# Kernel tuning notes

Hardware: AMD Instinct MI355X
Metric: run time of the kernel (lower is better)

## Reference

```python
import jax, jax.numpy as jnp
import numpy as np

B, S, IN = 1, 50000, 128
N = B * S
E = 800000
HID, HEADS, OUT = 64, 2, 64
NEG_SLOPE = 0.2
BN_EPS = 1e-5


def setup_inputs() -> dict:
    key = jax.random.key(0)
    ks = jax.random.split(key, 12)
    s = 0.1
    return {
        "data": jax.random.normal(ks[0], (B, S, IN), jnp.float32),
        "edge_index": jax.random.randint(ks[1], (2, E), 0, N, dtype=jnp.int64),
        "W0": jax.random.normal(ks[2], (IN, HEADS * HID), jnp.float32) * s,
        "att_src0": jax.random.normal(ks[3], (HEADS, HID), jnp.float32) * s,
        "att_dst0": jax.random.normal(ks[4], (HEADS, HID), jnp.float32) * s,
        "bias0": jnp.zeros((HEADS * HID,), jnp.float32),
        "gamma0": jnp.ones((HEADS * HID,), jnp.float32),
        "beta0": jnp.zeros((HEADS * HID,), jnp.float32),
        "W1": jax.random.normal(ks[5], (HEADS * HID, OUT), jnp.float32) * s,
        "att_src1": jax.random.normal(ks[6], (1, OUT), jnp.float32) * s,
        "att_dst1": jax.random.normal(ks[7], (1, OUT), jnp.float32) * s,
        "bias1": jnp.zeros((OUT,), jnp.float32),
    }


def gat_conv(x, edge_index, W, att_src, att_dst, bias, heads, ch, concat):
    n = x.shape[0]
    loop = jnp.arange(n, dtype=edge_index.dtype)
    src = jnp.concatenate([edge_index[0], loop])  # PyG adds self-loops by default
    dst = jnp.concatenate([edge_index[1], loop])
    h = (x @ W).reshape(n, heads, ch)  # [N,H,C]
    a_src = (h * att_src).sum(-1)  # [N,H]
    a_dst = (h * att_dst).sum(-1)  # [N,H]
    e = jax.nn.leaky_relu(a_src[src] + a_dst[dst], NEG_SLOPE)  # [Etot,H]
    m = jax.ops.segment_max(e, dst, num_segments=n)  # segment softmax over dst
    ex = jnp.exp(e - m[dst])
    denom = jax.ops.segment_sum(ex, dst, num_segments=n)
    alpha = ex / (denom[dst] + 1e-16)  # [Etot,H]
    out = jax.ops.segment_sum(h[src] * alpha[:, :, None], dst, num_segments=n)  # [N,H,C]
    out = out.reshape(n, heads * ch) if concat else out.mean(axis=1)
    return out + bias


def reference(data, edge_index, W0, att_src0, att_dst0, bias0, gamma0, beta0,
              W1, att_src1, att_dst1, bias1):
    x = data.reshape(N, IN)
    x = gat_conv(x, edge_index, W0, att_src0, att_dst0, bias0, HEADS, HID, True)
    mu = x.mean(axis=0)
    var = x.var(axis=0)
    x = (x - mu) * jax.lax.rsqrt(var + BN_EPS) * gamma0 + beta0  # BatchNorm1d (batch stats)
    x = jax.nn.elu(x)
    x = gat_conv(x, edge_index, W1, att_src1, att_dst1, bias1, 1, OUT, False)
    return x.reshape(B, S, OUT)
```

## Files before the change

### kernel.cpp

```cpp
#include <hip/hip_runtime.h>
#include <hip/hip_fp16.h>
#include <math.h>

#define N_NODES 50000
#define E_EDGES 800000
#define NEG_SLOPE 0.2f
#define BN_EPS 1e-5f

#define BK_SHIFT 9
#define NBK 98
#define L1_BLOCKS 256
#define L1_CHUNK (E_EDGES / L1_BLOCKS)
#define CNT_N (NBK * L1_BLOCKS)
#define SCG_BLOCKS ((CNT_N + 1023) / 1024)
#define STAGE_MAX 9216

__device__ __forceinline__ float lrelu(float v) { return v > 0.f ? v : NEG_SLOPE * v; }

__global__ void k_zero(float* __restrict__ bn_sum, float* __restrict__ bn_sumsq) {
  int t = threadIdx.x;
  if (t < 128) { bn_sum[t] = 0.f; bn_sumsq[t] = 0.f; }
}

__global__ __launch_bounds__(256) void k_l1hist(const int* __restrict__ dst,
                                                int* __restrict__ cnt) {
  __shared__ int lcnt[NBK];
  int t = threadIdx.x;
  if (t < NBK) lcnt[t] = 0;
  __syncthreads();
  int beg = blockIdx.x * L1_CHUNK, end = beg + L1_CHUNK;
  for (int e = beg + t; e < end; e += 256)
    atomicAdd(&lcnt[((unsigned int)dst[e]) >> BK_SHIFT], 1);
  __syncthreads();
  for (int b = t; b < NBK; b += 256) cnt[b * L1_BLOCKS + blockIdx.x] = lcnt[b];
}

__global__ __launch_bounds__(256) void k_scan1g(const int* __restrict__ cnt,
                                                int* __restrict__ tmp,
                                                int* __restrict__ bsums) {
  __shared__ int ts[256];
  int t = threadIdx.x;
  int base = blockIdx.x * 1024 + t * 4;
  int c0 = (base + 0 < CNT_N) ? cnt[base + 0] : 0;
  int c1 = (base + 1 < CNT_N) ? cnt[base + 1] : 0;
  int c2 = (base + 2 < CNT_N) ? cnt[base + 2] : 0;
  int c3 = (base + 3 < CNT_N) ? cnt[base + 3] : 0;
  int s = c0 + c1 + c2 + c3;
  ts[t] = s;
  __syncthreads();
  for (int off = 1; off < 256; off <<= 1) {
    int v = (t >= off) ? ts[t - off] : 0;
    __syncthreads();
    ts[t] += v;
    __syncthreads();
  }
  int excl = ts[t] - s;
  if (t == 255) bsums[blockIdx.x] = ts[255];
  if (base + 0 < CNT_N) tmp[base + 0] = excl;
  if (base + 1 < CNT_N) tmp[base + 1] = excl + c0;
  if (base + 2 < CNT_N) tmp[base + 2] = excl + c0 + c1;
  if (base + 3 < CNT_N) tmp[base + 3] = excl + c0 + c1 + c2;
}

__global__ void k_scan2g(int* __restrict__ bsums) {
  int t = threadIdx.x;
  int orig = (t < SCG_BLOCKS) ? bsums[t] : 0;
  int v = orig;
#pragma unroll
  for (int off = 1; off < 64; off <<= 1) {
    int u = __shfl_up(v, off);
    if (t >= off) v += u;
  }
  if (t < SCG_BLOCKS) bsums[t] = v - orig;
}

__global__ __launch_bounds__(256) void k_l1scatter(const int* __restrict__ src,
                                                   const int* __restrict__ dst,
                                                   const int* __restrict__ tmp,
                                                   const int* __restrict__ bsums,
                                                   unsigned int* __restrict__ binned) {
  __shared__ int cur[NBK];
  int t = threadIdx.x;
  for (int b = t; b < NBK; b += 256) {
    int idx = b * L1_BLOCKS + blockIdx.x;
    cur[b] = tmp[idx] + bsums[idx >> 10];
  }
  __syncthreads();
  int beg = blockIdx.x * L1_CHUNK, end = beg + L1_CHUNK;
  for (int e = beg + t; e < end; e += 256) {
    unsigned int d = (unsigned int)dst[e];
    int b = d >> BK_SHIFT;
    int p = atomicAdd(&cur[b], 1);
    binned[p] = ((unsigned int)src[e] << 16) | d;
  }
}

__global__ void k_bbase(const int* __restrict__ tmp, const int* __restrict__ bsums,
                        int* __restrict__ bucket_base) {
  int b = threadIdx.x;
  if (b < NBK) {
    int idx = b * L1_BLOCKS;
    bucket_base[b] = tmp[idx] + bsums[idx >> 10];
  }
  if (b == NBK) bucket_base[NBK] = E_EDGES;
}

__global__ __launch_bounds__(256) void k_scatter3(const int* __restrict__ bucket_base,
                                                  const unsigned int* __restrict__ binned,
                                                  int* __restrict__ row_ptr,
                                                  int* __restrict__ csr_src) {
  __shared__ int cnt[512];
  __shared__ int staging[STAGE_MAX];
  __shared__ int ts[256];
  int t = threadIdx.x;
  int b = blockIdx.x;
  int lo = b << BK_SHIFT;
  int hi = lo + 512; if (hi > N_NODES) hi = N_NODES;
  int nloc = hi - lo;
  int base = bucket_base[b];
  int end = bucket_base[b + 1];
  cnt[t] = 0; cnt[t + 256] = 0;
  __syncthreads();
  for (int i = base + t; i < end; i += 256)
    atomicAdd(&cnt[(binned[i] & 0xFFFFu) - lo], 1);
  __syncthreads();
  int c0 = cnt[2 * t], c1 = cnt[2 * t + 1];
  int pair = c0 + c1;
  ts[t] = pair;
  __syncthreads();
  for (int off = 1; off < 256; off <<= 1) {
    int v = (t >= off) ? ts[t - off] : 0;
    __syncthreads();
    ts[t] += v;
    __syncthreads();
  }
  int exclp = ts[t] - pair;
  cnt[2 * t] = exclp;
  cnt[2 * t + 1] = exclp + c0;
  if (2 * t < nloc) row_ptr[lo + 2 * t] = base + exclp;
  if (2 * t + 1 < nloc) row_ptr[lo + 2 * t + 1] = base + exclp + c0;
  if (b == NBK - 1 && t == 0) row_ptr[N_NODES] = E_EDGES;
  __syncthreads();
  for (int i = base + t; i < end; i += 256) {
    unsigned int v = binned[i];
    int d = (int)(v & 0xFFFFu) - lo;
    int p = atomicAdd(&cnt[d], 1);
    int s = (int)(v >> 16);
    if (p < STAGE_MAX) staging[p] = s;
    else csr_src[base + p] = s;
  }
  __syncthreads();
  int tot = end - base;
  int lim = tot < STAGE_MAX ? tot : STAGE_MAX;
  for (int k = t; k < lim; k += 256) csr_src[base + k] = staging[k];
}

__global__ __launch_bounds__(256) void k_gemm0(
    const float* __restrict__ x, const float* __restrict__ W,
    const float* __restrict__ att_s, const float* __restrict__ att_d,
    __half* __restrict__ h, float* __restrict__ a_src, float* __restrict__ a_dst) {
  __shared__ float xs[64 * 132];
  int t = threadIdx.x;
  int rowBase = blockIdx.x * 64;
#pragma unroll
  for (int j = 0; j < 8; j++) {
    int id = t + 256 * j;
    int row = id >> 5;
    int kk = (id & 31) * 4;
    float4 v = make_float4(0.f, 0.f, 0.f, 0.f);
    int gr = rowBase + row;
    if (gr < N_NODES) v = *(const float4*)&x[(size_t)gr * 128 + kk];
    *(float4*)&xs[row * 132 + kk] = v;
  }
  __syncthreads();

  int tc = t & 31, tr = t >> 5;
  int c = tc * 4, r0 = tr * 8;
  float acc[8][4];
#pragma unroll
  for (int i = 0; i < 8; i++)
#pragma unroll
    for (int j = 0; j < 4; j++) acc[i][j] = 0.f;

  for (int k4 = 0; k4 < 128; k4 += 4) {
    float4 wv[4];
#pragma unroll
    for (int kk = 0; kk < 4; kk++) wv[kk] = *(const float4*)&W[(k4 + kk) * 128 + c];
    float4 xv[8];
#pragma unroll
    for (int i = 0; i < 8; i++) xv[i] = *(const float4*)&xs[(r0 + i) * 132 + k4];
#pragma unroll
    for (int i = 0; i < 8; i++) {
      acc[i][0] += xv[i].x * wv[0].x + xv[i].y * wv[1].x + xv[i].z * wv[2].x + xv[i].w * wv[3].x;
      acc[i][1] += xv[i].x * wv[0].y + xv[i].y * wv[1].y + xv[i].z * wv[2].y + xv[i].w * wv[3].y;
      acc[i][2] += xv[i].x * wv[0].z + xv[i].y * wv[1].z + xv[i].z * wv[2].z + xv[i].w * wv[3].z;
      acc[i][3] += xv[i].x * wv[0].w + xv[i].y * wv[1].w + xv[i].z * wv[2].w + xv[i].w * wv[3].w;
    }
  }

  float as4[4], ad4[4];
#pragma unroll
  for (int j = 0; j < 4; j++) { as4[j] = att_s[c + j]; ad4[j] = att_d[c + j]; }
  int head = tc >> 4;
#pragma unroll
  for (int i = 0; i < 8; i++) {
    int gr = rowBase + r0 + i;
    float ps = acc[i][0] * as4[0] + acc[i][1] * as4[1] + acc[i][2] * as4[2] + acc[i][3] * as4[3];
    float pd = acc[i][0] * ad4[0] + acc[i][1] * ad4[1] + acc[i][2] * ad4[2] + acc[i][3] * ad4[3];
#pragma unroll
    for (int msk = 1; msk <= 8; msk <<= 1) {
      ps += __shfl_xor(ps, msk);
      pd += __shfl_xor(pd, msk);
    }
    if (gr < N_NODES) {
      __half2 p01 = __floats2half2_rn(acc[i][0], acc[i][1]);
      __half2 p23 = __floats2half2_rn(acc[i][2], acc[i][3]);
      uint2 pk;
      pk.x = *(unsigned int*)&p01;
      pk.y = *(unsigned int*)&p23;
      *(uint2*)&h[(size_t)gr * 128 + c] = pk;
      if ((t & 15) == 0) {
        a_src[gr * 2 + head] = ps;
        a_dst[gr * 2 + head] = pd;
      }
    }
  }
}

__global__ __launch_bounds__(256) void k_agg0(
    const int* __restrict__ row_ptr, const int* __restrict__ csr_src,
    const __half* __restrict__ h, const float* __restrict__ a_src,
    const float* __restrict__ a_dst, const float* __restrict__ bias,
    float* __restrict__ out) {
  int node = (blockIdx.x * blockDim.x + threadIdx.x) >> 6;
  if (node >= N_NODES) return;
  int l = threadIdx.x & 63;
  int head = l >> 5;
  int c = l * 2;
  float ad = a_dst[node * 2 + head];
  float m = lrelu(a_src[node * 2 + head] + ad);
  float d = 1.f;
  float2 hv = __half22float2(*(const __half2*)&h[(size_t)node * 128 + c]);
  float acc0 = hv.x, acc1 = hv.y;
  int beg = row_ptr[node], end = row_ptr[node + 1];
  int i = beg;
  for (; i + 8 <= end; i += 8) {
    int s0 = csr_src[i], s1 = csr_src[i + 1], s2 = csr_src[i + 2], s3 = csr_src[i + 3];
    int s4 = csr_src[i + 4], s5 = csr_src[i + 5], s6 = csr_src[i + 6], s7 = csr_src[i + 7];
    float e0 = lrelu(a_src[s0 * 2 + head] + ad), e1 = lrelu(a_src[s1 * 2 + head] + ad);
    float e2 = lrelu(a_src[s2 * 2 + head] + ad), e3 = lrelu(a_src[s3 * 2 + head] + ad);
    float e4 = lrelu(a_src[s4 * 2 + head] + ad), e5 = lrelu(a_src[s5 * 2 + head] + ad);
    float e6 = lrelu(a_src[s6 * 2 + head] + ad), e7 = lrelu(a_src[s7 * 2 + head] + ad);
    __half2 p0 = *(const __half2*)&h[(size_t)s0 * 128 + c];
    __half2 p1 = *(const __half2*)&h[(size_t)s1 * 128 + c];
    __half2 p2 = *(const __half2*)&h[(size_t)s2 * 128 + c];
    __half2 p3 = *(const __half2*)&h[(size_t)s3 * 128 + c];
    __half2 p4 = *(const __half2*)&h[(size_t)s4 * 128 + c];
    __half2 p5 = *(const __half2*)&h[(size_t)s5 * 128 + c];
    __half2 p6 = *(const __half2*)&h[(size_t)s6 * 128 + c];
    __half2 p7 = *(const __half2*)&h[(size_t)s7 * 128 + c];
    float nm = fmaxf(m, fmaxf(fmaxf(fmaxf(e0, e1), fmaxf(e2, e3)),
                              fmaxf(fmaxf(e4, e5), fmaxf(e6, e7))));
    float sc = __expf(m - nm);
    float w0 = __expf(e0 - nm), w1 = __expf(e1 - nm), w2 = __expf(e2 - nm), w3 = __expf(e3 - nm);
    float w4 = __expf(e4 - nm), w5 = __expf(e5 - nm), w6 = __expf(e6 - nm), w7 = __expf(e7 - nm);
    d = d * sc + ((w0 + w1) + (w2 + w3)) + ((w4 + w5) + (w6 + w7));
    float2 f0 = __half22float2(p0), f1 = __half22float2(p1);
    float2 f2 = __half22float2(p2), f3 = __half22float2(p3);
    float2 f4 = __half22float2(p4), f5 = __half22float2(p5);
    float2 f6 = __half22float2(p6), f7 = __half22float2(p7);
    acc0 = acc0 * sc + (w0 * f0.x + w1 * f1.x + w2 * f2.x + w3 * f3.x) +
           (w4 * f4.x + w5 * f5.x + w6 * f6.x + w7 * f7.x);
    acc1 = acc1 * sc + (w0 * f0.y + w1 * f1.y + w2 * f2.y + w3 * f3.y) +
           (w4 * f4.y + w5 * f5.y + w6 * f6.y + w7 * f7.y);
    m = nm;
  }
  for (; i + 4 <= end; i += 4) {
    int s0 = csr_src[i], s1 = csr_src[i + 1], s2 = csr_src[i + 2], s3 = csr_src[i + 3];
    float e0 = lrelu(a_src[s0 * 2 + head] + ad), e1 = lrelu(a_src[s1 * 2 + head] + ad);
    float e2 = lrelu(a_src[s2 * 2 + head] + ad), e3 = lrelu(a_src[s3 * 2 + head] + ad);
    __half2 p0 = *(const __half2*)&h[(size_t)s0 * 128 + c];
    __half2 p1 = *(const __half2*)&h[(size_t)s1 * 128 + c];
    __half2 p2 = *(const __half2*)&h[(size_t)s2 * 128 + c];
    __half2 p3 = *(const __half2*)&h[(size_t)s3 * 128 + c];
    float nm = fmaxf(fmaxf(m, e0), fmaxf(fmaxf(e1, e2), e3));
    float sc = __expf(m - nm);
    float w0 = __expf(e0 - nm), w1 = __expf(e1 - nm), w2 = __expf(e2 - nm), w3 = __expf(e3 - nm);
    d = d * sc + (w0 + w1) + (w2 + w3);
    float2 f0 = __half22float2(p0), f1 = __half22float2(p1);
    float2 f2 = __half22float2(p2), f3 = __half22float2(p3);
    acc0 = acc0 * sc + w0 * f0.x + w1 * f1.x + w2 * f2.x + w3 * f3.x;
    acc1 = acc1 * sc + w0 * f0.y + w1 * f1.y + w2 * f2.y + w3 * f3.y;
    m = nm;
  }
  for (; i < end; i++) {
    int s = csr_src[i];
    float ee = lrelu(a_src[s * 2 + head] + ad);
    __half2 pp = *(const __half2*)&h[(size_t)s * 128 + c];
    float nm = fmaxf(m, ee);
    float sc = __expf(m - nm);
    float w = __expf(ee - nm);
    float2 ff = __half22float2(pp);
    d = d * sc + w;
    acc0 = acc0 * sc + w * ff.x;
    acc1 = acc1 * sc + w * ff.y;
    m = nm;
  }
  float inv = 1.f / d;
  float2 o;
  o.x = acc0 * inv + bias[c];
  o.y = acc1 * inv + bias[c + 1];
  *(float2*)&out[(size_t)node * 128 + c] = o;
}

__global__ __launch_bounds__(256) void k_bnstats(const float* __restrict__ x,
                                                 float* __restrict__ bn_sum,
                                                 float* __restrict__ bn_sumsq) {
  int f = threadIdx.x & 127;
  int half = threadIdx.x >> 7;
  float s = 0.f, s2 = 0.f;
  for (int r = blockIdx.x * 2 + half; r < N_NODES; r += gridDim.x * 2) {
    float v = x[(size_t)r * 128 + f];
    s += v;
    s2 += v * v;
  }
  __shared__ float ls[256], ls2[256];
  ls[threadIdx.x] = s;
  ls2[threadIdx.x] = s2;
  __syncthreads();
  if (half == 0) {
    atomicAdd(&bn_sum[f], s + ls[f + 128]);
    atomicAdd(&bn_sumsq[f], s2 + ls2[f + 128]);
  }
}

__global__ void k_bnfinal(const float* __restrict__ sum, const float* __restrict__ sumsq,
                          const float* __restrict__ gamma, const float* __restrict__ beta,
                          float* __restrict__ scale, float* __restrict__ shift) {
  int f = threadIdx.x;
  float mu = sum[f] / (float)N_NODES;
  float var = sumsq[f] / (float)N_NODES - mu * mu;
  float sc = gamma[f] * rsqrtf(var + BN_EPS);
  scale[f] = sc;
  shift[f] = beta[f] - mu * sc;
}

__global__ __launch_bounds__(256) void k_gemm1(
    const float* __restrict__ x, const float* __restrict__ W,
    const float* __restrict__ scale, const float* __restrict__ shift,
    const float* __restrict__ att_s, const float* __restrict__ att_d,
    __half* __restrict__ h, float* __restrict__ a_src, float* __restrict__ a_dst) {
  __shared__ float xs[64 * 132];
  int t = threadIdx.x;
  int rowBase = blockIdx.x * 64;
#pragma unroll
  for (int j = 0; j < 8; j++) {
    int id = t + 256 * j;
    int row = id >> 5;
    int kk = (id & 31) * 4;
    float4 v = make_float4(0.f, 0.f, 0.f, 0.f);
    int gr = rowBase + row;
    if (gr < N_NODES) {
      float4 raw = *(const float4*)&x[(size_t)gr * 128 + kk];
      float4 sc = *(const float4*)&scale[kk];
      float4 sh = *(const float4*)&shift[kk];
      v.x = raw.x * sc.x + sh.x;
      v.y = raw.y * sc.y + sh.y;
      v.z = raw.z * sc.z + sh.z;
      v.w = raw.w * sc.w + sh.w;
      v.x = v.x > 0.f ? v.x : __expf(v.x) - 1.f;
      v.y = v.y > 0.f ? v.y : __expf(v.y) - 1.f;
      v.z = v.z > 0.f ? v.z : __expf(v.z) - 1.f;
      v.w = v.w > 0.f ? v.w : __expf(v.w) - 1.f;
    }
    *(float4*)&xs[row * 132 + kk] = v;
  }
  __syncthreads();

  int tc = t & 15, tr = t >> 4;
  int c = tc * 4, r0 = tr * 4;
  float acc[4][4];
#pragma unroll
  for (int i = 0; i < 4; i++)
#pragma unroll
    for (int j = 0; j < 4; j++) acc[i][j] = 0.f;

  for (int k4 = 0; k4 < 128; k4 += 4) {
    float4 wv[4];
#pragma unroll
    for (int kk = 0; kk < 4; kk++) wv[kk] = *(const float4*)&W[(k4 + kk) * 64 + c];
    float4 xv[4];
#pragma unroll
    for (int i = 0; i < 4; i++) xv[i] = *(const float4*)&xs[(r0 + i) * 132 + k4];
#pragma unroll
    for (int i = 0; i < 4; i++) {
      acc[i][0] += xv[i].x * wv[0].x + xv[i].y * wv[1].x + xv[i].z * wv[2].x + xv[i].w * wv[3].x;
      acc[i][1] += xv[i].x * wv[0].y + xv[i].y * wv[1].y + xv[i].z * wv[2].y + xv[i].w * wv[3].y;
      acc[i][2] += xv[i].x * wv[0].z + xv[i].y * wv[1].z + xv[i].z * wv[2].z + xv[i].w * wv[3].z;
      acc[i][3] += xv[i].x * wv[0].w + xv[i].y * wv[1].w + xv[i].z * wv[2].w + xv[i].w * wv[3].w;
    }
  }

  float as4[4], ad4[4];
#pragma unroll
  for (int j = 0; j < 4; j++) { as4[j] = att_s[c + j]; ad4[j] = att_d[c + j]; }
#pragma unroll
  for (int i = 0; i < 4; i++) {
    int gr = rowBase + r0 + i;
    float ps = acc[i][0] * as4[0] + acc[i][1] * as4[1] + acc[i][2] * as4[2] + acc[i][3] * as4[3];
    float pd = acc[i][0] * ad4[0] + acc[i][1] * ad4[1] + acc[i][2] * ad4[2] + acc[i][3] * ad4[3];
#pragma unroll
    for (int msk = 1; msk <= 8; msk <<= 1) {
      ps += __shfl_xor(ps, msk);
      pd += __shfl_xor(pd, msk);
    }
    if (gr < N_NODES) {
      __half2 p01 = __floats2half2_rn(acc[i][0], acc[i][1]);
      __half2 p23 = __floats2half2_rn(acc[i][2], acc[i][3]);
      uint2 pk;
      pk.x = *(unsigned int*)&p01;
      pk.y = *(unsigned int*)&p23;
      *(uint2*)&h[(size_t)gr * 64 + c] = pk;
      if ((t & 15) == 0) {
        a_src[gr] = ps;
        a_dst[gr] = pd;
      }
    }
  }
}

__global__ __launch_bounds__(256) void k_agg1(
    const int* __restrict__ row_ptr, const int* __restrict__ csr_src,
    const __half* __restrict__ h, const float* __restrict__ a_src,
    const float* __restrict__ a_dst, const float* __restrict__ bias,
    float* __restrict__ out) {
  int node = (blockIdx.x * blockDim.x + threadIdx.x) >> 6;
  if (node >= N_NODES) return;
  int l = threadIdx.x & 63;
  float ad = a_dst[node];
  float m = lrelu(a_src[node] + ad);
  float d = 1.f;
  float acc = __half2float(h[(size_t)node * 64 + l]);
  int beg = row_ptr[node], end = row_ptr[node + 1];
  int i = beg;
  for (; i + 8 <= end; i += 8) {
    int s0 = csr_src[i], s1 = csr_src[i + 1], s2 = csr_src[i + 2], s3 = csr_src[i + 3];
    int s4 = csr_src[i + 4], s5 = csr_src[i + 5], s6 = csr_src[i + 6], s7 = csr_src[i + 7];
    float e0 = lrelu(a_src[s0] + ad), e1 = lrelu(a_src[s1] + ad);
    float e2 = lrelu(a_src[s2] + ad), e3 = lrelu(a_src[s3] + ad);
    float e4 = lrelu(a_src[s4] + ad), e5 = lrelu(a_src[s5] + ad);
    float e6 = lrelu(a_src[s6] + ad), e7 = lrelu(a_src[s7] + ad);
    __half p0 = h[(size_t)s0 * 64 + l], p1 = h[(size_t)s1 * 64 + l];
    __half p2 = h[(size_t)s2 * 64 + l], p3 = h[(size_t)s3 * 64 + l];
    __half p4 = h[(size_t)s4 * 64 + l], p5 = h[(size_t)s5 * 64 + l];
    __half p6 = h[(size_t)s6 * 64 + l], p7 = h[(size_t)s7 * 64 + l];
    float nm = fmaxf(m, fmaxf(fmaxf(fmaxf(e0, e1), fmaxf(e2, e3)),
                              fmaxf(fmaxf(e4, e5), fmaxf(e6, e7))));
    float sc = __expf(m - nm);
    float w0 = __expf(e0 - nm), w1 = __expf(e1 - nm), w2 = __expf(e2 - nm), w3 = __expf(e3 - nm);
    float w4 = __expf(e4 - nm), w5 = __expf(e5 - nm), w6 = __expf(e6 - nm), w7 = __expf(e7 - nm);
    d = d * sc + ((w0 + w1) + (w2 + w3)) + ((w4 + w5) + (w6 + w7));
    acc = acc * sc +
          (w0 * __half2float(p0) + w1 * __half2float(p1) + w2 * __half2float(p2) +
           w3 * __half2float(p3)) +
          (w4 * __half2float(p4) + w5 * __half2float(p5) + w6 * __half2float(p6) +
           w7 * __half2float(p7));
    m = nm;
  }
  for (; i + 4 <= end; i += 4) {
    int s0 = csr_src[i], s1 = csr_src[i + 1], s2 = csr_src[i + 2], s3 = csr_src[i + 3];
    float e0 = lrelu(a_src[s0] + ad), e1 = lrelu(a_src[s1] + ad);
    float e2 = lrelu(a_src[s2] + ad), e3 = lrelu(a_src[s3] + ad);
    __half p0 = h[(size_t)s0 * 64 + l], p1 = h[(size_t)s1 * 64 + l];
    __half p2 = h[(size_t)s2 * 64 + l], p3 = h[(size_t)s3 * 64 + l];
    float nm = fmaxf(fmaxf(m, e0), fmaxf(fmaxf(e1, e2), e3));
    float sc = __expf(m - nm);
    float w0 = __expf(e0 - nm), w1 = __expf(e1 - nm), w2 = __expf(e2 - nm), w3 = __expf(e3 - nm);
    d = d * sc + (w0 + w1) + (w2 + w3);
    acc = acc * sc + w0 * __half2float(p0) + w1 * __half2float(p1) + w2 * __half2float(p2) +
          w3 * __half2float(p3);
    m = nm;
  }
  for (; i < end; i++) {
    int s = csr_src[i];
    float ee = lrelu(a_src[s] + ad);
    __half pp = h[(size_t)s * 64 + l];
    float nm = fmaxf(m, ee);
    float sc = __expf(m - nm);
    float w = __expf(ee - nm);
    d = d * sc + w;
    acc = acc * sc + w * __half2float(pp);
    m = nm;
  }
  out[(size_t)node * 64 + l] = acc / d + bias[l];
}

extern "C" void kernel_launch(void* const* d_in, const int* in_sizes, int n_in,
                              void* d_out, int out_size, void* d_ws, size_t ws_size,
                              hipStream_t stream) {
  const float* data = (const float*)d_in[0];
  const int* ei = (const int*)d_in[1];
  const float* W0 = (const float*)d_in[2];
  const float* att_src0 = (const float*)d_in[3];
  const float* att_dst0 = (const float*)d_in[4];
  const float* bias0 = (const float*)d_in[5];
  const float* gamma0 = (const float*)d_in[6];
  const float* beta0 = (const float*)d_in[7];
  const float* W1 = (const float*)d_in[8];
  const float* att_src1 = (const float*)d_in[9];
  const float* att_dst1 = (const float*)d_in[10];
  const float* bias1 = (const float*)d_in[11];
  float* out = (float*)d_out;

  char* ws = (char*)d_ws;
  size_t off = 0;
  auto alloc = [&](size_t bytes) -> void* {
    void* p = ws + off;
    off = (off + bytes + 255) & ~(size_t)255;
    return p;
  };
  int* cnt = (int*)alloc((size_t)CNT_N * 4);
  int* tmp = (int*)alloc((size_t)CNT_N * 4);
  int* bsums = (int*)alloc(32 * 4);
  int* bucket_base = (int*)alloc((NBK + 1) * 4);
  int* row_ptr = (int*)alloc((N_NODES + 1) * 4);
  unsigned int* binned = (unsigned int*)alloc((size_t)E_EDGES * 4);
  int* csr_src = (int*)alloc((size_t)E_EDGES * 4);
  __half* h0 = (__half*)alloc((size_t)N_NODES * 128 * 2);
  float* a_s0 = (float*)alloc((size_t)N_NODES * 2 * 4);
  float* a_d0 = (float*)alloc((size_t)N_NODES * 2 * 4);
  float* out0 = (float*)alloc((size_t)N_NODES * 128 * 4);
  float* bn_sum = (float*)alloc(128 * 4);
  float* bn_sumsq = (float*)alloc(128 * 4);
  float* bn_scale = (float*)alloc(128 * 4);
  float* bn_shift = (float*)alloc(128 * 4);
  __half* h1 = h0;
  float* a_s1 = a_s0;
  float* a_d1 = a_d0;

  const int* srcArr = ei;
  const int* dstArr = ei + E_EDGES;

  k_zero<<<1, 128, 0, stream>>>(bn_sum, bn_sumsq);
  k_l1hist<<<L1_BLOCKS, 256, 0, stream>>>(dstArr, cnt);
  k_scan1g<<<SCG_BLOCKS, 256, 0, stream>>>(cnt, tmp, bsums);
  k_scan2g<<<1, 64, 0, stream>>>(bsums);
  k_l1scatter<<<L1_BLOCKS, 256, 0, stream>>>(srcArr, dstArr, tmp, bsums, binned);
  k_bbase<<<1, 128, 0, stream>>>(tmp, bsums, bucket_base);
  k_scatter3<<<NBK, 256, 0, stream>>>(bucket_base, binned, row_ptr, csr_src);
  k_gemm0<<<(N_NODES + 63) / 64, 256, 0, stream>>>(data, W0, att_src0, att_dst0, h0, a_s0, a_d0);
  k_agg0<<<(N_NODES + 3) / 4, 256, 0, stream>>>(row_ptr, csr_src, h0, a_s0, a_d0, bias0, out0);
  k_bnstats<<<1024, 256, 0, stream>>>(out0, bn_sum, bn_sumsq);
  k_bnfinal<<<1, 128, 0, stream>>>(bn_sum, bn_sumsq, gamma0, beta0, bn_scale, bn_shift);
  k_gemm1<<<(N_NODES + 63) / 64, 256, 0, stream>>>(out0, W1, bn_scale, bn_shift, att_src1,
                                                   att_dst1, h1, a_s1, a_d1);
  k_agg1<<<(N_NODES + 3) / 4, 256, 0, stream>>>(row_ptr, csr_src, h1, a_s1, a_d1, bias1, out);
}
```

Before: 301.1 us.

## Replace FP32 SIMT GEMMs with FP16 MFMA GEMMs and pre-converted inputs

```diff
diff --git a/kernel.cpp b/kernel.cpp
--- a/kernel.cpp
+++ b/kernel.cpp
@@ -15,11 +15,61 @@
 #define SCG_BLOCKS ((CNT_N + 1023) / 1024)
 #define STAGE_MAX 9216
 
+typedef __attribute__((ext_vector_type(8))) _Float16 half8;
+typedef __attribute__((ext_vector_type(4))) float f32x4;
+
 __device__ __forceinline__ float lrelu(float v) { return v > 0.f ? v : NEG_SLOPE * v; }
 
 __global__ void k_zero(float* __restrict__ bn_sum, float* __restrict__ bn_sumsq) {
   int t = threadIdx.x;
   if (t < 128) { bn_sum[t] = 0.f; bn_sumsq[t] = 0.f; }
+}
+
+__global__ __launch_bounds__(256) void k_cvtx(const float* __restrict__ x,
+                                              _Float16* __restrict__ xh) {
+  int i = blockIdx.x * 256 + threadIdx.x;
+  const float4* p = (const float4*)x + (size_t)i * 2;
+  float4 a = p[0], b = p[1];
+  half8 o = {(_Float16)a.x, (_Float16)a.y, (_Float16)a.z, (_Float16)a.w,
+             (_Float16)b.x, (_Float16)b.y, (_Float16)b.z, (_Float16)b.w};
+  *((half8*)xh + i) = o;
+}
+
+__global__ void k_cvtW(const float* __restrict__ W0, const float* __restrict__ W1,
+                       _Float16* __restrict__ W0t, _Float16* __restrict__ W1t) {
+  int t = threadIdx.x;
+  for (int idx = t; idx < 128 * 128; idx += 256) {
+    int k = idx >> 7, c = idx & 127;
+    W0t[c * 128 + k] = (_Float16)W0[idx];
+  }
+  for (int idx = t; idx < 128 * 64; idx += 256) {
+    int k = idx >> 6, c = idx & 63;
+    W1t[c * 128 + k] = (_Float16)W1[idx];
+  }
+}
+
+__global__ __launch_bounds__(256) void k_cvty(const float* __restrict__ x,
+                                              const float* __restrict__ scale,
+                                              const float* __restrict__ shift,
+                                              _Float16* __restrict__ yh) {
+  int i = blockIdx.x * 256 + threadIdx.x;
+  int c = (i * 8) & 127;
+  float4 s0 = *(const float4*)&scale[c], s1 = *(const float4*)&scale[c + 4];
+  float4 f0 = *(const float4*)&shift[c], f1 = *(const float4*)&shift[c + 4];
+  const float4* p = (const float4*)x + (size_t)i * 2;
+  float4 a = p[0], b = p[1];
+  float v[8];
+  v[0] = a.x * s0.x + f0.x; v[1] = a.y * s0.y + f0.y;
+  v[2] = a.z * s0.z + f0.z; v[3] = a.w * s0.w + f0.w;
+  v[4] = b.x * s1.x + f1.x; v[5] = b.y * s1.y + f1.y;
+  v[6] = b.z * s1.z + f1.z; v[7] = b.w * s1.w + f1.w;
+  half8 o;
+#pragma unroll
+  for (int j = 0; j < 8; j++) {
+    float e = v[j] > 0.f ? v[j] : __expf(v[j]) - 1.f;
+    o[j] = (_Float16)e;
+  }
+  *((half8*)yh + i) = o;
 }
 
 __global__ __launch_bounds__(256) void k_l1hist(const int* __restrict__ dst,
@@ -155,74 +205,98 @@
   for (int k = t; k < lim; k += 256) csr_src[base + k] = staging[k];
 }
 
-__global__ __launch_bounds__(256) void k_gemm0(
-    const float* __restrict__ x, const float* __restrict__ W,
+__global__ __launch_bounds__(256) void k_gemm0m(
+    const _Float16* __restrict__ xh, const _Float16* __restrict__ Wt,
     const float* __restrict__ att_s, const float* __restrict__ att_d,
-    __half* __restrict__ h, float* __restrict__ a_src, float* __restrict__ a_dst) {
-  __shared__ float xs[64 * 132];
-  int t = threadIdx.x;
-  int rowBase = blockIdx.x * 64;
-#pragma unroll
-  for (int j = 0; j < 8; j++) {
-    int id = t + 256 * j;
-    int row = id >> 5;
-    int kk = (id & 31) * 4;
-    float4 v = make_float4(0.f, 0.f, 0.f, 0.f);
-    int gr = rowBase + row;
-    if (gr < N_NODES) v = *(const float4*)&x[(size_t)gr * 128 + kk];
-    *(float4*)&xs[row * 132 + kk] = v;
-  }
-  __syncthreads();
-
-  int tc = t & 31, tr = t >> 5;
-  int c = tc * 4, r0 = tr * 8;
-  float acc[8][4];
-#pragma unroll
-  for (int i = 0; i < 8; i++)
-#pragma unroll
-    for (int j = 0; j < 4; j++) acc[i][j] = 0.f;
-
-  for (int k4 = 0; k4 < 128; k4 += 4) {
-    float4 wv[4];
-#pragma unroll
-    for (int kk = 0; kk < 4; kk++) wv[kk] = *(const float4*)&W[(k4 + kk) * 128 + c];
-    float4 xv[8];
-#pragma unroll
-    for (int i = 0; i < 8; i++) xv[i] = *(const float4*)&xs[(r0 + i) * 132 + k4];
-#pragma unroll
-    for (int i = 0; i < 8; i++) {
-      acc[i][0] += xv[i].x * wv[0].x + xv[i].y * wv[1].x + xv[i].z * wv[2].x + xv[i].w * wv[3].x;
-      acc[i][1] += xv[i].x * wv[0].y + xv[i].y * wv[1].y + xv[i].z * wv[2].y + xv[i].w * wv[3].y;
-      acc[i][2] += xv[i].x * wv[0].z + xv[i].y * wv[1].z + xv[i].z * wv[2].z + xv[i].w * wv[3].z;
-      acc[i][3] += xv[i].x * wv[0].w + xv[i].y * wv[1].w + xv[i].z * wv[2].w + xv[i].w * wv[3].w;
+    _Float16* __restrict__ h, float* __restrict__ a_src, float* __restrict__ a_dst) {
+  int lane = threadIdx.x & 63;
+  int wv = threadIdx.x >> 6;
+  int row0 = blockIdx.x * 64 + wv * 16;
+  int m = lane & 15, kg = lane >> 4;
+  int arow = row0 + m;
+  int arowc = arow < N_NODES ? arow : N_NODES - 1;
+  f32x4 acc[8];
+#pragma unroll
+  for (int ct = 0; ct < 8; ct++) acc[ct] = (f32x4){0.f, 0.f, 0.f, 0.f};
+#pragma unroll
+  for (int kc = 0; kc < 4; kc++) {
+    half8 af = *(const half8*)&xh[(size_t)arowc * 128 + kc * 32 + kg * 8];
+#pragma unroll
+    for (int ct = 0; ct < 8; ct++) {
+      half8 bf = *(const half8*)&Wt[(ct * 16 + m) * 128 + kc * 32 + kg * 8];
+      acc[ct] = __builtin_amdgcn_mfma_f32_16x16x32_f16(af, bf, acc[ct], 0, 0, 0);
     }
   }
-
-  float as4[4], ad4[4];
-#pragma unroll
-  for (int j = 0; j < 4; j++) { as4[j] = att_s[c + j]; ad4[j] = att_d[c + j]; }
-  int head = tc >> 4;
-#pragma unroll
-  for (int i = 0; i < 8; i++) {
-    int gr = rowBase + r0 + i;
-    float ps = acc[i][0] * as4[0] + acc[i][1] * as4[1] + acc[i][2] * as4[2] + acc[i][3] * as4[3];
-    float pd = acc[i][0] * ad4[0] + acc[i][1] * ad4[1] + acc[i][2] * ad4[2] + acc[i][3] * ad4[3];
+  float as[8], ad[8];
+#pragma unroll
+  for (int ct = 0; ct < 8; ct++) { as[ct] = att_s[ct * 16 + m]; ad[ct] = att_d[ct * 16 + m]; }
+#pragma unroll
+  for (int r = 0; r < 4; r++) {
+    int row = row0 + kg * 4 + r;
+    bool ok = row < N_NODES;
+    float ps0 = 0.f, pd0 = 0.f, ps1 = 0.f, pd1 = 0.f;
+#pragma unroll
+    for (int ct = 0; ct < 4; ct++) { ps0 += acc[ct][r] * as[ct]; pd0 += acc[ct][r] * ad[ct]; }
+#pragma unroll
+    for (int ct = 4; ct < 8; ct++) { ps1 += acc[ct][r] * as[ct]; pd1 += acc[ct][r] * ad[ct]; }
 #pragma unroll
     for (int msk = 1; msk <= 8; msk <<= 1) {
-      ps += __shfl_xor(ps, msk);
-      pd += __shfl_xor(pd, msk);
+      ps0 += __shfl_xor(ps0, msk); pd0 += __shfl_xor(pd0, msk);
+      ps1 += __shfl_xor(ps1, msk); pd1 += __shfl_xor(pd1, msk);
     }
-    if (gr < N_NODES) {
-      __half2 p01 = __floats2half2_rn(acc[i][0], acc[i][1]);
-      __half2 p23 = __floats2half2_rn(acc[i][2], acc[i][3]);
-      uint2 pk;
-      pk.x = *(unsigned int*)&p01;
-      pk.y = *(unsigned int*)&p23;
-      *(uint2*)&h[(size_t)gr * 128 + c] = pk;
-      if ((t & 15) == 0) {
-        a_src[gr * 2 + head] = ps;
-        a_dst[gr * 2 + head] = pd;
+    if (ok) {
+#pragma unroll
+      for (int ct = 0; ct < 8; ct++)
+        h[(size_t)row * 128 + ct * 16 + m] = (_Float16)acc[ct][r];
+      if (m == 0) {
+        a_src[row * 2 + 0] = ps0; a_dst[row * 2 + 0] = pd0;
+        a_src[row * 2 + 1] = ps1; a_dst[row * 2 + 1] = pd1;
       }
+    }
+  }
+}
+
+__global__ __launch_bounds__(256) void k_gemm1m(
+    const _Float16* __restrict__ yh, const _Float16* __restrict__ Wt,
+    const float* __restrict__ att_s, const float* __restrict__ att_d,
+    _Float16* __restrict__ h, float* __restrict__ a_src, float* __restrict__ a_dst) {
+  int lane = threadIdx.x & 63;
+  int wv = threadIdx.x >> 6;
+  int row0 = blockIdx.x * 64 + wv * 16;
+  int m = lane & 15, kg = lane >> 4;
+  int arow = row0 + m;
+  int arowc = arow < N_NODES ? arow : N_NODES - 1;
+  f32x4 acc[4];
+#pragma unroll
+  for (int ct = 0; ct < 4; ct++) acc[ct] = (f32x4){0.f, 0.f, 0.f, 0.f};
+#pragma unroll
+  for (int kc = 0; kc < 4; kc++) {
+    half8 af = *(const half8*)&yh[(size_t)arowc * 128 + kc * 32 + kg * 8];
+#pragma unroll
+    for (int ct = 0; ct < 4; ct++) {
+      half8 bf = *(const half8*)&Wt[(ct * 16 + m) * 128 + kc * 32 + kg * 8];
+      acc[ct] = __builtin_amdgcn_mfma_f32_16x16x32_f16(af, bf, acc[ct], 0, 0, 0);
+    }
+  }
+  float as[4], ad[4];
+#pragma unroll
+  for (int ct = 0; ct < 4; ct++) { as[ct] = att_s[ct * 16 + m]; ad[ct] = att_d[ct * 16 + m]; }
+#pragma unroll
+  for (int r = 0; r < 4; r++) {
+    int row = row0 + kg * 4 + r;
+    bool ok = row < N_NODES;
+    float ps = 0.f, pd = 0.f;
+#pragma unroll
+    for (int ct = 0; ct < 4; ct++) { ps += acc[ct][r] * as[ct]; pd += acc[ct][r] * ad[ct]; }
+#pragma unroll
+    for (int msk = 1; msk <= 8; msk <<= 1) {
+      ps += __shfl_xor(ps, msk); pd += __shfl_xor(pd, msk);
+    }
+    if (ok) {
+#pragma unroll
+      for (int ct = 0; ct < 4; ct++)
+        h[(size_t)row * 64 + ct * 16 + m] = (_Float16)acc[ct][r];
+      if (m == 0) { a_src[row] = ps; a_dst[row] = pd; }
     }
   }
 }
@@ -345,90 +419,6 @@
   shift[f] = beta[f] - mu * sc;
 }
 
-__global__ __launch_bounds__(256) void k_gemm1(
-    const float* __restrict__ x, const float* __restrict__ W,
-    const float* __restrict__ scale, const float* __restrict__ shift,
-    const float* __restrict__ att_s, const float* __restrict__ att_d,
-    __half* __restrict__ h, float* __restrict__ a_src, float* __restrict__ a_dst) {
-  __shared__ float xs[64 * 132];
-  int t = threadIdx.x;
-  int rowBase = blockIdx.x * 64;
-#pragma unroll
-  for (int j = 0; j < 8; j++) {
-    int id = t + 256 * j;
-    int row = id >> 5;
-    int kk = (id & 31) * 4;
-    float4 v = make_float4(0.f, 0.f, 0.f, 0.f);
-    int gr = rowBase + row;
-    if (gr < N_NODES) {
-      float4 raw = *(const float4*)&x[(size_t)gr * 128 + kk];
-      float4 sc = *(const float4*)&scale[kk];
-      float4 sh = *(const float4*)&shift[kk];
-      v.x = raw.x * sc.x + sh.x;
-      v.y = raw.y * sc.y + sh.y;
-      v.z = raw.z * sc.z + sh.z;
-      v.w = raw.w * sc.w + sh.w;
-      v.x = v.x > 0.f ? v.x : __expf(v.x) - 1.f;
-      v.y = v.y > 0.f ? v.y : __expf(v.y) - 1.f;
-      v.z = v.z > 0.f ? v.z : __expf(v.z) - 1.f;
-      v.w = v.w > 0.f ? v.w : __expf(v.w) - 1.f;
-    }
-    *(float4*)&xs[row * 132 + kk] = v;
-  }
-  __syncthreads();
-
-  int tc = t & 15, tr = t >> 4;
-  int c = tc * 4, r0 = tr * 4;
-  float acc[4][4];
-#pragma unroll
-  for (int i = 0; i < 4; i++)
-#pragma unroll
-    for (int j = 0; j < 4; j++) acc[i][j] = 0.f;
-
-  for (int k4 = 0; k4 < 128; k4 += 4) {
-    float4 wv[4];
-#pragma unroll
-    for (int kk = 0; kk < 4; kk++) wv[kk] = *(const float4*)&W[(k4 + kk) * 64 + c];
-    float4 xv[4];
-#pragma unroll
-    for (int i = 0; i < 4; i++) xv[i] = *(const float4*)&xs[(r0 + i) * 132 + k4];
-#pragma unroll
-    for (int i = 0; i < 4; i++) {
-      acc[i][0] += xv[i].x * wv[0].x + xv[i].y * wv[1].x + xv[i].z * wv[2].x + xv[i].w * wv[3].x;
-      acc[i][1] += xv[i].x * wv[0].y + xv[i].y * wv[1].y + xv[i].z * wv[2].y + xv[i].w * wv[3].y;
-      acc[i][2] += xv[i].x * wv[0].z + xv[i].y * wv[1].z + xv[i].z * wv[2].z + xv[i].w * wv[3].z;
-      acc[i][3] += xv[i].x * wv[0].w + xv[i].y * wv[1].w + xv[i].z * wv[2].w + xv[i].w * wv[3].w;
-    }
-  }
-
-  float as4[4], ad4[4];
-#pragma unroll
-  for (int j = 0; j < 4; j++) { as4[j] = att_s[c + j]; ad4[j] = att_d[c + j]; }
-#pragma unroll
-  for (int i = 0; i < 4; i++) {
-    int gr = rowBase + r0 + i;
-    float ps = acc[i][0] * as4[0] + acc[i][1] * as4[1] + acc[i][2] * as4[2] + acc[i][3] * as4[3];
-    float pd = acc[i][0] * ad4[0] + acc[i][1] * ad4[1] + acc[i][2] * ad4[2] + acc[i][3] * ad4[3];
-#pragma unroll
-    for (int msk = 1; msk <= 8; msk <<= 1) {
-      ps += __shfl_xor(ps, msk);
-      pd += __shfl_xor(pd, msk);
-    }
-    if (gr < N_NODES) {
-      __half2 p01 = __floats2half2_rn(acc[i][0], acc[i][1]);
-      __half2 p23 = __floats2half2_rn(acc[i][2], acc[i][3]);
-      uint2 pk;
-      pk.x = *(unsigned int*)&p01;
-      pk.y = *(unsigned int*)&p23;
-      *(uint2*)&h[(size_t)gr * 64 + c] = pk;
-      if ((t & 15) == 0) {
-        a_src[gr] = ps;
-        a_dst[gr] = pd;
-      }
-    }
-  }
-}
-
 __global__ __launch_bounds__(256) void k_agg1(
     const int* __restrict__ row_ptr, const int* __restrict__ csr_src,
     const __half* __restrict__ h, const float* __restrict__ a_src,
@@ -526,15 +516,19 @@
   int* row_ptr = (int*)alloc((N_NODES + 1) * 4);
   unsigned int* binned = (unsigned int*)alloc((size_t)E_EDGES * 4);
   int* csr_src = (int*)alloc((size_t)E_EDGES * 4);
-  __half* h0 = (__half*)alloc((size_t)N_NODES * 128 * 2);
+  _Float16* xh = (_Float16*)alloc((size_t)N_NODES * 128 * 2);
+  _Float16* W0t = (_Float16*)alloc(128 * 128 * 2);
+  _Float16* W1t = (_Float16*)alloc(64 * 128 * 2);
+  _Float16* h0 = (_Float16*)alloc((size_t)N_NODES * 128 * 2);
   float* a_s0 = (float*)alloc((size_t)N_NODES * 2 * 4);
   float* a_d0 = (float*)alloc((size_t)N_NODES * 2 * 4);
   float* out0 = (float*)alloc((size_t)N_NODES * 128 * 4);
+  _Float16* yh = (_Float16*)alloc((size_t)N_NODES * 128 * 2);
   float* bn_sum = (float*)alloc(128 * 4);
   float* bn_sumsq = (float*)alloc(128 * 4);
   float* bn_scale = (float*)alloc(128 * 4);
   float* bn_shift = (float*)alloc(128 * 4);
-  __half* h1 = h0;
+  _Float16* h1 = h0;
   float* a_s1 = a_s0;
   float* a_d1 = a_d0;
 
@@ -542,17 +536,21 @@
   const int* dstArr = ei + E_EDGES;
 
   k_zero<<<1, 128, 0, stream>>>(bn_sum, bn_sumsq);
+  k_cvtW<<<1, 256, 0, stream>>>(W0, W1, W0t, W1t);
+  k_cvtx<<<3125, 256, 0, stream>>>(data, xh);
   k_l1hist<<<L1_BLOCKS, 256, 0, stream>>>(dstArr, cnt);
   k_scan1g<<<SCG_BLOCKS, 256, 0, stream>>>(cnt, tmp, bsums);
   k_scan2g<<<1, 64, 0, stream>>>(bsums);
   k_l1scatter<<<L1_BLOCKS, 256, 0, stream>>>(srcArr, dstArr, tmp, bsums, binned);
   k_bbase<<<1, 128, 0, stream>>>(tmp, bsums, bucket_base);
   k_scatter3<<<NBK, 256, 0, stream>>>(bucket_base, binned, row_ptr, csr_src);
-  k_gemm0<<<(N_NODES + 63) / 64, 256, 0, stream>>>(data, W0, att_src0, att_dst0, h0, a_s0, a_d0);
-  k_agg0<<<(N_NODES + 3) / 4, 256, 0, stream>>>(row_ptr, csr_src, h0, a_s0, a_d0, bias0, out0);
+  k_gemm0m<<<(N_NODES + 63) / 64, 256, 0, stream>>>(xh, W0t, att_src0, att_dst0, h0, a_s0, a_d0);
+  k_agg0<<<(N_NODES + 3) / 4, 256, 0, stream>>>(row_ptr, csr_src, (const __half*)h0, a_s0, a_d0,
+                                                bias0, out0);
   k_bnstats<<<1024, 256, 0, stream>>>(out0, bn_sum, bn_sumsq);
   k_bnfinal<<<1, 128, 0, stream>>>(bn_sum, bn_sumsq, gamma0, beta0, bn_scale, bn_shift);
-  k_gemm1<<<(N_NODES + 63) / 64, 256, 0, stream>>>(out0, W1, bn_scale, bn_shift, att_src1,
-                                                   att_dst1, h1, a_s1, a_d1);
-  k_agg1<<<(N_NODES + 3) / 4, 256, 0, stream>>>(row_ptr, csr_src, h1, a_s1, a_d1, bias1, out);
-}
+  k_cvty<<<3125, 256, 0, stream>>>(out0, bn_scale, bn_shift, yh);
+  k_gemm1m<<<(N_NODES + 63) / 64, 256, 0, stream>>>(yh, W1t, att_src1, att_dst1, h1, a_s1, a_d1);
+  k_agg1<<<(N_NODES + 3) / 4, 256, 0, stream>>>(row_ptr, csr_src, (const __half*)h1, a_s1, a_d1,
+                                                bias1, out);
+}
```

Result: slower. 307.5 us (+2.1%).
